# Kernel tuning notes

Hardware: AMD Instinct MI355X
Metric: run time of the kernel (lower is better)

Reference implementation:

```python
import jax, jax.numpy as jnp
import numpy as np

DN = ('NCHW', 'OIHW', 'NCHW')

def conv(x, w, b, stride=1, pad=0):
    y = jax.lax.conv_general_dilated(x, w, (stride, stride), ((pad, pad), (pad, pad)), dimension_numbers=DN)
    return y + b[None, :, None, None]

def maxpool(x, k, s):
    return jax.lax.reduce_window(x, -jnp.inf, jax.lax.max, (1, 1, k, k), (1, 1, s, s), 'VALID')

def bilinear_resize(x, oh, ow):
    # torch F.interpolate(mode='bilinear', align_corners=False)
    H, W = x.shape[2], x.shape[3]
    def grid(n_in, n_out):
        c = (jnp.arange(n_out, dtype=x.dtype) + 0.5) * (n_in / n_out) - 0.5
        c = jnp.clip(c, 0.0, n_in - 1)
        lo = jnp.floor(c).astype(jnp.int32)
        hi = jnp.minimum(lo + 1, n_in - 1)
        return lo, hi, c - lo
    r0, r1, wr = grid(H, oh)
    c0, c1, wc = grid(W, ow)
    top = x[:, :, r0, :] * (1 - wr)[None, None, :, None] + x[:, :, r1, :] * wr[None, None, :, None]
    return top[:, :, :, c0] * (1 - wc) + top[:, :, :, c1] * wc

def setup_inputs():
    key = jax.random.key(0)
    ks = jax.random.split(key, 18)
    s = 0.02
    d = {}
    d['x'] = jax.random.normal(ks[0], (16, 3, 448, 448), jnp.float32)
    d['w1'] = jax.random.normal(ks[1], (64, 3, 7, 7), jnp.float32) * s
    d['b1'] = jax.random.normal(ks[2], (64,), jnp.float32) * s
    d['w3'] = jax.random.normal(ks[3], (192, 64, 3, 3), jnp.float32) * s
    d['b3'] = jax.random.normal(ks[4], (192,), jnp.float32) * s
    d['w4'] = jax.random.normal(ks[5], (256, 192, 3, 3), jnp.float32) * s
    d['b4'] = jax.random.normal(ks[6], (256,), jnp.float32) * s
    d['w7'] = jax.random.normal(ks[7], (512, 256, 2, 2), jnp.float32) * s
    d['b7'] = jax.random.normal(ks[8], (512,), jnp.float32) * s
    d['w8'] = jax.random.normal(ks[9], (1024, 512, 2, 2), jnp.float32) * s
    d['b8'] = jax.random.normal(ks[10], (1024,), jnp.float32) * s
    d['wu'] = jax.random.normal(ks[11], (1024, 1024, 2, 2), jnp.float32) * s
    d['bu'] = jax.random.normal(ks[12], (1024,), jnp.float32) * s
    d['lc_w'] = jax.random.normal(ks[13], (1024, 256, 7, 7, 3, 3), jnp.float32) * s
    d['lc_b'] = jax.random.normal(ks[14], (256, 7, 7), jnp.float32) * s
    d['fc_w'] = jax.random.normal(ks[15], (4949, 12544), jnp.float32) * s  # S*S*(C+B*5)=7*7*101
    d['fc_b'] = jax.random.normal(ks[16], (4949,), jnp.float32) * s
    return d

def reference(x, w1, b1, w3, b3, w4, b4, w7, b7, w8, b8, wu, bu, lc_w, lc_b, fc_w, fc_b):
    x = conv(x, w1, b1, 2, 3)        # [B,64,224,224]
    x = maxpool(x, 2, 2)             # 112
    x = conv(x, w3, b3, 1, 1)        # [B,192,112,112]
    x = maxpool(x, 2, 2)             # 56
    x = conv(x, w4, b4)              # [B,256,54,54]
    x = maxpool(x, 2, 2)             # 27
    # CombinedNet backbone not defined in source listing: identity (256->256)
    x = conv(x, w7, b7)              # [B,512,26,26]
    x = maxpool(x, 2, 2)             # 13
    x = conv(x, w8, b8)              # [B,1024,12,12]
    x = conv(x, wu, bu)              # 11 (ultblock applied twice, shared weights)
    x = conv(x, wu, bu)              # 10
    x = maxpool(x, 5, 4)             # [B,1024,2,2]
    x = x[:, :, :14, :14]
    x = bilinear_resize(x, 7, 7)     # [B,1024,7,7]
    # LocallyConnected2d(1024,256,7,7,k=3,s=1,p=1) without materializing the unfold*weight product
    B = x.shape[0]
    xp = jnp.pad(x, ((0, 0), (0, 0), (1, 1), (1, 1)))
    patches = jnp.stack([xp[:, :, i:i + 7, j:j + 7] for i in range(3) for j in range(3)], axis=2)
    patches = patches.reshape(B, 1024, 3, 3, 7, 7)  # [B,C,kh,kw,H,W]
    y = jnp.einsum('bcijhw,cohwij->bohw', patches, lc_w) + lc_b[None]
    y = jnp.where(y > 0, y, 0.1 * y)  # LeakyReLU(0.1)
    # Dropout(p=0.5) is identity at inference; Linear
    y = y.reshape(B, -1) @ fc_w.T + fc_b  # [B,4949]
    return y.reshape(B, 7, 7, 101)
```

## Files before the change

kernel.cpp:

```cpp
#include <hip/hip_runtime.h>

#define UNR _Pragma("unroll")

typedef __attribute__((ext_vector_type(8))) short short8v;
typedef __attribute__((ext_vector_type(4))) float f32x4;

__device__ __forceinline__ ushort f2bf(float f) {
    union { float f; unsigned u; } x; x.f = f;
    unsigned r = (x.u + 0x7fffu + ((x.u >> 16) & 1u)) >> 16;
    return (ushort)r;
}
__device__ __forceinline__ float bf2f(ushort u) {
    union { unsigned u; float f; } x; x.u = ((unsigned)u) << 16;
    return x.f;
}

__device__ __forceinline__ void gll16(const ushort* gp, ushort* lp) {
    __builtin_amdgcn_global_load_lds(
        (const __attribute__((address_space(1))) unsigned int*)(const void*)gp,
        (__attribute__((address_space(3))) unsigned int*)(void*)lp, 16, 0, 0);
}

template<int Wp,int Hp,int OW,int OH,int WpN,int HpN,int PADN,int CN,int WAVES>
__global__ __launch_bounds__(WAVES*64)
void convc1(const ushort* __restrict__ Xp, const ushort* __restrict__ Wb,
            const float* __restrict__ bias, ushort* __restrict__ Yp)
{
    constexpr int CIN = 4, STRIDE = 2, NSTEP = 7;
    constexpr int POW = OW/2, POH = OH/2;
    constexpr int NTOT = 16*POW*POH*4;

    const int lane = (int)threadIdx.x & 63;
    const int wave = (int)threadIdx.x >> 6;
    const int n0   = (blockIdx.y*WAVES + wave) * 64;
    const int lm   = lane & 15;
    const int lk   = lane >> 4;

    int ns[4];
    unsigned boff[4];
    UNR for (int nf=0; nf<4; ++nf) {
        int n = n0 + nf*16 + lm;
        if (n > NTOT-1) n = NTOT-1;
        ns[nf] = n;
        int q = n & 3, pp = n >> 2;
        int px = pp % POW; int t = pp / POW;
        int py = t % POH;  int b = t / POH;
        int oy = 2*py + (q>>1), ox = 2*px + (q&1);
        boff[nf] = ((unsigned)(b*Hp + oy*STRIDE)*Wp + (unsigned)(ox*STRIDE))*CIN
                 + 8u*lk;
    }

    f32x4 acc[4][4];
    UNR for (int i=0;i<4;++i) UNR for (int j=0;j<4;++j) acc[i][j] = f32x4{0.f,0.f,0.f,0.f};

    auto ldfr = [&](int s, short8v (&a)[4], short8v (&bf)[4]) {
        const unsigned xoff = (unsigned)(s*Wp*CIN);
        UNR for (int mf=0; mf<4; ++mf)
            a[mf] = *(const short8v*)(Wb + (unsigned)((s*4 + mf)<<9) + (unsigned)lane*8);
        UNR for (int nf=0; nf<4; ++nf)
            bf[nf] = *(const short8v*)(Xp + boff[nf] + xoff);
    };
    auto dm = [&](short8v (&a)[4], short8v (&bf)[4]) {
        UNR for (int mf=0; mf<4; ++mf)
            UNR for (int nf=0; nf<4; ++nf)
                acc[mf][nf] = __builtin_amdgcn_mfma_f32_16x16x32_bf16(
                                  a[mf], bf[nf], acc[mf][nf], 0, 0, 0);
    };

    short8v aA[4], bA[4], aB[4], bB[4];
    ldfr(0, aA, bA);
    for (int sb = 0; sb < NSTEP; sb += 2) {
        if (sb+1 < NSTEP) ldfr(sb+1, aB, bB);
        dm(aA, bA);
        if (sb+2 < NSTEP) ldfr(sb+2, aA, bA);
        if (sb+1 < NSTEP) dm(aB, bB);
    }

    UNR for (int mf=0; mf<4; ++mf) {
        const int co = mf*16 + 4*lk;
        f32x4 bi = *(const f32x4*)(bias + co);
        UNR for (int nf=0; nf<4; ++nf) {
            f32x4 v = acc[mf][nf];
            UNR for (int r=0;r<4;++r) {
                float t2 = v[r] + bi[r];
                t2 = fmaxf(t2, __shfl_xor(t2, 1, 64));
                t2 = fmaxf(t2, __shfl_xor(t2, 2, 64));
                v[r] = t2;
            }
            if ((lane & 3) == 0 && (n0 + nf*16 + lm) < NTOT) {
                int pp = ns[nf] >> 2;
                int px = pp % POW; int t2 = pp / POW;
                int py = t2 % POH; int b = t2 / POH;
                unsigned off = ((unsigned)(b*HpN + py + PADN)*WpN
                                + (unsigned)(px + PADN))*CN + co;
                ushort4 s; s.x=f2bf(v[0]); s.y=f2bf(v[1]); s.z=f2bf(v[2]); s.w=f2bf(v[3]);
                *(ushort4*)(Yp + off) = s;
            }
        }
    }
}

template<int CIN,int K,int STRIDE,int Wp,int Hp,int OW,int OH,int COUT,
         bool POOL,int WpN,int HpN,int PADN,int CN,int MT,int NT,int SPLITS,
         int LINX=0,int LINY=0>
__global__ __launch_bounds__(256)
void convt(const ushort* __restrict__ Xp, const ushort* __restrict__ Wb,
           const float* __restrict__ bias, ushort* __restrict__ Yp,
           float* __restrict__ part)
{
    static_assert(MT*NT == 4, "4 waves");
    constexpr int POW = OW/2, POH = OH/2;
    constexpr int NTOT = POOL ? 16*POW*POH*4 : 16*OW*OH;
    constexpr int NCH = CIN/32, NSTEP = K*K*NCH;
    constexpr int SPS = NSTEP/SPLITS;
    constexpr int CA = MT*4, CB = NT*4, CPW = MT + NT;

    int bx, by;
    if constexpr (LINX > 0) {
        constexpr int CHUNK = LINX*LINY/8;
        int bid = (int)blockIdx.x;
        int p = (bid & 7)*CHUNK + (bid >> 3);
        bx = p % LINX; by = p / LINX;
    } else {
        bx = (int)blockIdx.x; by = (int)blockIdx.y;
    }

    const int t    = (int)threadIdx.x;
    const int lane = t & 63;
    const int w    = t >> 6;
    const int mr   = w / NT, nc = w % NT;
    const int cy0  = bx * MT;
    const int n0b  = by * (NT*64);
    const int nw0  = n0b + nc*64;
    const int lm   = lane & 15, lk = lane >> 4;
    const int s0   = blockIdx.z * SPS, sE = s0 + SPS;

    __shared__ __align__(1024) ushort Ab[2][CA*512];
    __shared__ __align__(1024) ushort Bb[2][CB*512];

    auto nmap = [&](int n, int& b, int& oy, int& ox) {
        if (n > NTOT-1) n = NTOT-1;
        if constexpr (POOL) {
            int q = n & 3, pp = n >> 2;
            int px = pp % POW; int tt = pp / POW;
            int py = tt % POH;  b = tt / POH;
            oy = 2*py + (q>>1); ox = 2*px + (q&1);
        } else {
            ox = n % OW; int tt = n / OW; oy = tt % OH; b = tt / OH;
        }
    };

    int ns[4];
    UNR for (int nf=0; nf<4; ++nf) {
        int n = nw0 + nf*16 + lm;
        if (n > NTOT-1) n = NTOT-1;
        ns[nf] = n;
    }

    unsigned bsrc[CPW];
    UNR for (int j=0; j<CPW; ++j) {
        int q = w*CPW + j;
        if (q >= CA) {
            int bq = q - CA;
            int n = n0b + bq*16 + (lane >> 2);
            int b, oy, ox; nmap(n, b, oy, ox);
            bsrc[j] = ((unsigned)(b*Hp + oy*STRIDE)*Wp + (unsigned)(ox*STRIDE))*CIN
                    + (unsigned)(lane & 3)*8u;
        } else bsrc[j] = 0;
    }

    auto xoffs = [&](int s) -> unsigned {
        int c0  = (s % NCH)*32;
        int kxy = s / NCH;
        int kx  = kxy % K, ky = kxy / K;
        return (unsigned)((ky*Wp + kx)*CIN + c0);
    };
    auto stage = [&](int s, int buf) {
        const unsigned xoff = xoffs(s);
        UNR for (int j=0; j<CPW; ++j) {
            int q = w*CPW + j;
            if (q < CA) {
                const ushort* src = Wb
                    + ((size_t)(((cy0 + (q>>2))*NSTEP + s)*4 + (q&3)) << 9)
                    + (unsigned)lane*8;
                gll16(src, &Ab[buf][(unsigned)q*512u + (unsigned)lane*8u]);
            } else {
                gll16(Xp + bsrc[j] + xoff,
                      &Bb[buf][(unsigned)(q-CA)*512u + (unsigned)lane*8u]);
            }
        }
    };

    f32x4 acc[4][4];
    UNR for (int i=0;i<4;++i) UNR for (int j=0;j<4;++j) acc[i][j] = f32x4{0.f,0.f,0.f,0.f};

    auto compute = [&](int buf) {
        short8v a[4], bf[4];
        UNR for (int mf=0; mf<4; ++mf)
            a[mf] = *(const short8v*)&Ab[buf][(unsigned)((mr*4+mf)*64 + lane)*8u];
        UNR for (int nf=0; nf<4; ++nf)
            bf[nf] = *(const short8v*)&Bb[buf][(unsigned)((nc*64 + nf*16 + lm)*4 + lk)*8u];
        __builtin_amdgcn_s_setprio(1);
        UNR for (int mf=0; mf<4; ++mf)
            UNR for (int nf=0; nf<4; ++nf)
                acc[mf][nf] = __builtin_amdgcn_mfma_f32_16x16x32_bf16(
                                  a[mf], bf[nf], acc[mf][nf], 0, 0, 0);
        __builtin_amdgcn_s_setprio(0);
    };

    stage(s0, 0);
    __syncthreads();
    int buf = 0;
    for (int s = s0; s < sE; ++s) {
        if (s+1 < sE) stage(s+1, buf^1);
        compute(buf);
        __syncthreads();
        buf ^= 1;
    }

    UNR for (int mf=0; mf<4; ++mf) {
        const int co = (cy0 + mr)*64 + mf*16 + 4*lk;
        if constexpr (SPLITS > 1) {
            UNR for (int nf=0; nf<4; ++nf) {
                if ((nw0 + nf*16 + lm) < NTOT)
                    *(f32x4*)(part + ((size_t)blockIdx.z*NTOT + ns[nf])*COUT + co)
                        = acc[mf][nf];
            }
        } else {
            f32x4 bi = *(const f32x4*)(bias + co);
            UNR for (int nf=0; nf<4; ++nf) {
                f32x4 v = acc[mf][nf];
                UNR for (int r=0;r<4;++r) v[r] += bi[r];
                if constexpr (POOL) {
                    UNR for (int r=0;r<4;++r) {
                        float tt = v[r];
                        tt = fmaxf(tt, __shfl_xor(tt, 1, 64));
                        tt = fmaxf(tt, __shfl_xor(tt, 2, 64));
                        v[r] = tt;
                    }
                    if ((lane & 3) == 0 && (nw0 + nf*16 + lm) < NTOT) {
                        int pp = ns[nf] >> 2;
                        int px = pp % POW; int t2 = pp / POW;
                        int py = t2 % POH; int b = t2 / POH;
                        unsigned off = ((unsigned)(b*HpN + py + PADN)*WpN
                                        + (unsigned)(px + PADN))*CN + co;
                        ushort4 s2; s2.x=f2bf(v[0]); s2.y=f2bf(v[1]); s2.z=f2bf(v[2]); s2.w=f2bf(v[3]);
                        *(ushort4*)(Yp + off) = s2;
                    }
                } else {
                    if ((nw0 + nf*16 + lm) < NTOT) {
                        int n = ns[nf];
                        int ox = n % OW; int t2 = n / OW; int oy = t2 % OH; int b = t2 / OH;
                        unsigned off = ((unsigned)(b*HpN + oy)*WpN + (unsigned)ox)*CN + co;
                        ushort4 s2; s2.x=f2bf(v[0]); s2.y=f2bf(v[1]); s2.z=f2bf(v[2]); s2.w=f2bf(v[3]);
                        *(ushort4*)(Yp + off) = s2;
                    }
                }
            }
        }
    }
}

template<int COUT,int OW,int OH,int WpN,int HpN,int CN,int SPLITS>
__global__ void kreduce(const float* __restrict__ part, const float* __restrict__ bias,
                        ushort* __restrict__ Yp) {
    constexpr int NTOT = 16*OW*OH;
    int idx = blockIdx.x*256 + (int)threadIdx.x;
    if (idx >= NTOT*COUT) return;
    int co = idx % COUT; int n = idx / COUT;
    float sum = 0.f;
    UNR for (int ks=0; ks<SPLITS; ++ks)
        sum += part[((size_t)ks*NTOT + n)*COUT + co];
    sum += bias[co];
    int ox = n % OW; int t = n / OW; int oy = t % OH; int b = t / OH;
    Yp[((unsigned)(b*HpN + oy)*WpN + (unsigned)ox)*CN + co] = f2bf(sum);
}

__global__ void x1build(const float* __restrict__ x, ushort* __restrict__ X1) {
    int idx = blockIdx.x*256 + (int)threadIdx.x;
    int xx = idx % 456; int t = idx/456; int y = t % 456; int b = t/456;
    ushort4 s; s.x = 0; s.y = 0; s.z = 0; s.w = 0;
    if (xx >= 3 && xx < 451 && y >= 3 && y < 451) {
        const float* px = x + ((size_t)b*3*448 + (y-3))*448 + (xx-3);
        s.x = f2bf(px[0]); s.y = f2bf(px[200704]); s.z = f2bf(px[401408]);
    }
    *(ushort4*)(X1 + ((unsigned)(b*456 + y)*456 + (unsigned)xx)*4) = s;
}

__global__ void x3ring(ushort* __restrict__ X3) {
    int idx = blockIdx.x*256 + (int)threadIdx.x;
    if (idx >= 462848) return;
    int b = idx / 28928; int j = idx % 28928;
    unsigned off;
    if (j < 14592) {
        int r = j / 7296; int rem = j % 7296;
        int y = r ? 113 : 0;
        off = ((unsigned)(b*114 + y)*114)*64u + (unsigned)rem;
    } else {
        int j2 = j - 14592;
        int y = 1 + j2/128;
        int rem = j2 % 128;
        int xx = (rem >> 6) ? 113 : 0;
        off = (((unsigned)(b*114 + y)*114) + (unsigned)xx)*64u + (unsigned)(rem & 63);
    }
    X3[off] = 0;
}

__global__ void wcvt1(const float* __restrict__ w, ushort* __restrict__ o) {
    int idx = blockIdx.x*256 + (int)threadIdx.x;
    if (idx >= 14336) return;
    int e = idx & 7; int t = idx >> 3;
    int lane = t & 63; t >>= 6;
    int mf = t & 3; int s = t >> 2;
    int co = mf*16 + (lane & 15);
    int cc = (lane >> 4)*8 + e;
    int kx = cc >> 2, ci = cc & 3;
    float v = 0.f;
    if (kx < 7 && ci < 3) v = w[(((size_t)co*3 + ci)*7 + s)*7 + kx];
    o[idx] = f2bf(v);
}

template<int CIN,int K,int COUT>
__global__ void wcvt(const float* __restrict__ w, ushort* __restrict__ o) {
    constexpr int NCH = CIN/32, NSTEP = K*K*NCH;
    int idx = blockIdx.x*256 + (int)threadIdx.x;
    if (idx >= COUT*K*K*CIN) return;
    int e = idx & 7; int t = idx >> 3;
    int lane = t & 63; t >>= 6;
    int mf = t & 3; t >>= 2;
    int s = t % NSTEP; int cy = t / NSTEP;
    int co = cy*64 + mf*16 + (lane & 15);
    int kxy = s / NCH, ch = s % NCH;
    int ci = ch*32 + (lane >> 4)*8 + e;
    int ky = kxy / K, kx = kxy % K;
    o[idx] = f2bf(w[(((size_t)co*CIN + ci)*K + ky)*K + kx]);
}

__global__ void pool54_k(const ushort* __restrict__ in, float* __restrict__ out) {
    int idx = blockIdx.x*256 + (int)threadIdx.x;
    int c = idx & 1023; int t = idx >> 10; int q = t & 3; int b = t >> 2;
    int i = q >> 1, j = q & 1;
    float m = -1e30f;
    UNR for (int r=0;r<5;++r)
        UNR for (int cc=0;cc<5;++cc)
            m = fmaxf(m, bf2f(in[(((unsigned)(b*10 + i*4+r))*10 + (unsigned)(j*4+cc))*1024 + c]));
    out[((size_t)(b*1024 + c))*4 + q] = m;
}

__device__ __forceinline__ void bigrid(int k, int& lo, float& f) {
    float c = ((float)k + 0.5f) * (2.0f/7.0f) - 0.5f;
    c = fminf(fmaxf(c, 0.f), 1.f);
    float fl = floorf(c);
    lo = (int)fl;
    f = c - fl;
}

__global__ void buildPb(const float* __restrict__ pp, ushort* __restrict__ Pb) {
    int idx = blockIdx.x*256 + (int)threadIdx.x;
    int k = idx & 15;
    int c = (idx >> 4) & 1023;
    int r = idx >> 14;
    int b = r & 15; int hw = r >> 4;
    float val = 0.f;
    if (k < 9) {
        int i = k/3, j = k%3;
        int h = hw/7, w2 = hw%7;
        int rr = h + i - 1, cc = w2 + j - 1;
        if (rr>=0 && rr<7 && cc>=0 && cc<7) {
            int rlo; float rf; bigrid(rr, rlo, rf);
            int clo; float cf; bigrid(cc, clo, cf);
            int rhi = min(rlo+1,1), chi = min(clo+1,1);
            const float* qq = pp + ((size_t)(b*1024 + c))*4;
            float v00=qq[rlo*2+clo], v01=qq[rlo*2+chi], v10=qq[rhi*2+clo], v11=qq[rhi*2+chi];
            float top = v00*(1.f-cf) + v01*cf;
            float bot = v10*(1.f-cf) + v11*cf;
            val = top*(1.f-rf) + bot*rf;
        }
    }
    Pb[idx] = f2bf(val);
}

__global__ __launch_bounds__(256)
void lconv_fused(const float* __restrict__ lcw, const ushort* __restrict__ Pb,
                 float* __restrict__ part) {
    const int bid = (int)blockIdx.x;
    const int xcd = bid & 7;
    const int i   = bid >> 3;
    const int hw  = i % 49;
    const int ks  = xcd + 8*(i/49);
    const int t   = (int)threadIdx.x;
    const int lane = t & 63, w = t >> 6;
    const int lm = lane & 15, lk = lane >> 4;
    const int c0 = ks*64;

    __shared__ ushort A[2][8192];

    auto ldreg = [&](int cc, float (&w9)[2][9]) {
        const int cb = c0 + cc*2;
        UNR for (int cl=0; cl<2; ++cl) {
            const float* src = lcw + ((size_t)(cb+cl)*256 + (unsigned)(w*64+lane))*441
                             + hw*9;
            __builtin_memcpy(w9[cl], src, 36);
        }
    };
    auto wrlds = [&](int buf, float (&w9)[2][9]) {
        UNR for (int cl=0; cl<2; ++cl) {
            int rem = cl*256 + w*64 + lane;
            ushort u[16];
            UNR for (int k=0;k<8;++k) u[k]=f2bf(w9[cl][k]);
            u[8]=f2bf(w9[cl][8]);
            UNR for (int k=9;k<16;++k) u[k]=0;
            *(short8v*)&A[buf][(unsigned)rem*8u] = *(short8v*)&u[0];
            *(short8v*)&A[buf][4096u + (unsigned)rem*8u] = *(short8v*)&u[8];
        }
    };

    f32x4 acc[4];
    UNR for (int q=0;q<4;++q) acc[q] = f32x4{0.f,0.f,0.f,0.f};

    const ushort* Bb = Pb + (size_t)(hw*16 + lm)*16384 + ks*1024 + lk*8;
    const int arow = (lk&1)*512 + (lk>>1)*256 + w*64 + lm;

    auto mmac = [&](int buf, int cc) {
        short8v bv = *(const short8v*)(Bb + cc*32);
        UNR for (int mf = 0; mf < 4; ++mf) {
            short8v av = *(const short8v*)&A[buf][(unsigned)(arow + mf*16)*8u];
            acc[mf] = __builtin_amdgcn_mfma_f32_16x16x32_bf16(av, bv, acc[mf], 0,0,0);
        }
    };

    float wA[2][9], wB[2][9];
    ldreg(0, wA);
    wrlds(0, wA);
    ldreg(1, wB);
    for (int cc = 0; cc < 32; cc += 2) {
        mmac(0, cc);
        wrlds(1, wB);
        if (cc+2 < 32) ldreg(cc+2, wA);
        mmac(1, cc+1);
        if (cc+2 < 32) {
            wrlds(0, wA);
            if (cc+3 < 32) ldreg(cc+3, wB);
        }
    }

    UNR for (int mf=0; mf<4; ++mf)
        UNR for (int r=0;r<4;++r) {
            int o = w*64 + mf*16 + 4*lk + r;
            part[(((size_t)ks*49 + hw)*256 + o)*16 + lm] = acc[mf][r];
        }
}

__global__ void lreduce2(const float* __restrict__ part, const float* __restrict__ lcb,
                         float* __restrict__ yact) {
    int idx = blockIdx.x*256 + (int)threadIdx.x;
    int b = idx & 15; int o = (idx >> 4) & 255; int hw = idx >> 12;
    float sum = 0.f;
    UNR for (int ks=0; ks<16; ++ks)
        sum += part[(((size_t)ks*49 + hw)*256 + o)*16 + b];
    sum += lcb[o*49 + hw];
    float v = (sum > 0.f) ? sum : 0.1f*sum;
    yact[b*12544 + o*49 + hw] = v;
}

__global__ __launch_bounds__(256)
void fc_k(const float* __restrict__ act, const float* __restrict__ fw,
          const float* __restrict__ fb, float* __restrict__ out) {
    __shared__ float alds[16][256];
    __shared__ float red[4][4][16];
    const int t = (int)threadIdx.x;
    const int o0 = blockIdx.x*4;
    float acc[4][16];
    UNR for (int oo=0;oo<4;++oo) UNR for (int b=0;b<16;++b) acc[oo][b]=0.f;

    for (int k0=0; k0<12544; k0+=256) {
        __syncthreads();
        UNR for (int b=0;b<16;++b) alds[b][t] = act[b*12544 + k0 + t];
        __syncthreads();
        float wv[4];
        UNR for (int oo=0;oo<4;++oo) {
            int o = o0+oo;
            wv[oo] = (o < 4949) ? fw[(size_t)o*12544 + k0 + t] : 0.f;
        }
        UNR for (int b=0;b<16;++b) {
            float av = alds[b][t];
            UNR for (int oo=0;oo<4;++oo) acc[oo][b] = fmaf(wv[oo], av, acc[oo][b]);
        }
    }
    UNR for (int oo=0;oo<4;++oo)
        UNR for (int b=0;b<16;++b) {
            float v = acc[oo][b];
            UNR for (int off=32; off; off>>=1) v += __shfl_xor(v, off, 64);
            acc[oo][b] = v;
        }
    const int wave = t>>6, lane = t&63;
    if (lane == 0)
        UNR for (int oo=0;oo<4;++oo)
            UNR for (int b=0;b<16;++b) red[wave][oo][b] = acc[oo][b];
    __syncthreads();
    if (t < 64) {
        int oo = t>>4, b = t&15;
        float v = red[0][oo][b]+red[1][oo][b]+red[2][oo][b]+red[3][oo][b];
        int o = o0+oo;
        if (o < 4949) out[b*4949 + o] = v + fb[o];
    }
}

extern "C" void kernel_launch(void* const* d_in, const int* in_sizes, int n_in,
                              void* d_out, int out_size, void* d_ws, size_t ws_size,
                              hipStream_t stream) {
    const float* x   = (const float*)d_in[0];
    const float* w1  = (const float*)d_in[1];
    const float* b1  = (const float*)d_in[2];
    const float* w3  = (const float*)d_in[3];
    const float* b3  = (const float*)d_in[4];
    const float* w4  = (const float*)d_in[5];
    const float* b4  = (const float*)d_in[6];
    const float* w7  = (const float*)d_in[7];
    const float* b7  = (const float*)d_in[8];
    const float* w8  = (const float*)d_in[9];
    const float* b8  = (const float*)d_in[10];
    const float* wu  = (const float*)d_in[11];
    const float* bu  = (const float*)d_in[12];
    const float* lcw = (const float*)d_in[13];
    const float* lcb = (const float*)d_in[14];
    const float* fw  = (const float*)d_in[15];
    const float* fb  = (const float*)d_in[16];
    float* out = (float*)d_out;

    char* base = (char*)d_ws;
    auto alloc = [&](size_t bytes) { char* p = base; base += (bytes + 255) & ~(size_t)255; return p; };
    ushort* X1  = (ushort*)alloc(16u*456*456*4*2);
    ushort* X3  = (ushort*)alloc(16u*114*114*64*2);
    ushort* X4  = (ushort*)alloc(16u*56*56*192*2);
    ushort* X7  = (ushort*)alloc(16u*27*27*256*2);
    ushort* X8  = (ushort*)alloc(16u*13*13*512*2);
    ushort* XU1 = (ushort*)alloc(16u*12*12*1024*2);
    ushort* XU2 = (ushort*)alloc(16u*11*11*1024*2);
    ushort* XU3 = (ushort*)alloc(16u*10*10*1024*2);
    ushort* W1b = (ushort*)alloc(64u*224*2);
    ushort* W3b = (ushort*)alloc(192u*576*2);
    ushort* W4b = (ushort*)alloc(256u*1728*2);
    ushort* W7b = (ushort*)alloc(512u*1024*2);
    ushort* W8b = (ushort*)alloc(1024u*2048*2);
    ushort* WUb = (ushort*)alloc(1024u*4096*2);
    float*  pp  = (float*)alloc(16u*1024*4*4);
    ushort* Pb  = (ushort*)alloc((size_t)49*16*16384*2);
    float*  part = (float*)alloc((size_t)16*49*256*16*4);
    float*  partK = (float*)alloc((size_t)4*2304*1024*4);
    float*  yact = (float*)X7;

    x1build<<<12996, 256, 0, stream>>>(x, X1);
    x3ring<<<1808, 256, 0, stream>>>(X3);
    wcvt1<<<56, 256, 0, stream>>>(w1, W1b);
    wcvt<64,3,192><<<432, 256, 0, stream>>>(w3, W3b);
    wcvt<192,3,256><<<1728, 256, 0, stream>>>(w4, W4b);
    wcvt<256,2,512><<<2048, 256, 0, stream>>>(w7, W7b);
    wcvt<512,2,1024><<<8192, 256, 0, stream>>>(w8, W8b);
    wcvt<1024,2,1024><<<16384, 256, 0, stream>>>(wu, WUb);

    convc1<456,456,224,224,114,114,1,64, 4>
        <<<dim3(1,3136), 256, 0, stream>>>(X1, W1b, b1, X3);
    convt<64,3,1,114,114,112,112,192, true,56,56,0,192, 1,4,1, 3,784>
        <<<2352, 256, 0, stream>>>(X3, W3b, b3, X4, nullptr);
    convt<192,3,1,56,56,54,54,256, true,27,27,0,256, 2,2,1>
        <<<dim3(2,365,1), 256, 0, stream>>>(X4, W4b, b4, X7, nullptr);
    convt<256,2,1,27,27,26,26,512, true,13,13,0,512, 2,2,1>
        <<<dim3(4,85,1), 256, 0, stream>>>(X7, W7b, b7, X8, nullptr);
    convt<512,2,1,13,13,12,12,1024, false,12,12,0,1024, 2,2,4>
        <<<dim3(8,18,4), 256, 0, stream>>>(X8, W8b, nullptr, nullptr, partK);
    kreduce<1024,12,12,12,12,1024,4><<<9216, 256, 0, stream>>>(partK, b8, XU1);
    convt<1024,2,1,12,12,11,11,1024, false,11,11,0,1024, 2,2,4>
        <<<dim3(8,16,4), 256, 0, stream>>>(XU1, WUb, nullptr, nullptr, partK);
    kreduce<1024,11,11,11,11,1024,4><<<7744, 256, 0, stream>>>(partK, bu, XU2);
    convt<1024,2,1,11,11,10,10,1024, false,10,10,0,1024, 2,2,4>
        <<<dim3(8,13,4), 256, 0, stream>>>(XU2, WUb, nullptr, nullptr, partK);
    kreduce<1024,10,10,10,10,1024,4><<<6400, 256, 0, stream>>>(partK, bu, XU3);

    pool54_k<<<256, 256, 0, stream>>>(XU3, pp);
    buildPb<<<50176, 256, 0, stream>>>(pp, Pb);
    lconv_fused<<<784, 256, 0, stream>>>(lcw, Pb, part);
    lreduce2<<<784, 256, 0, stream>>>(part, lcb, yact);
    fc_k<<<1238, 256, 0, stream>>>(yact, fw, fb, out);
}
```

Measured before the change: 784.9 us.

## Vectorize split-K reductions, XCD-aware block remap, and re-layout conv B staging

The split-K reduction kernels (kreduce, lreduce2) now have each thread handle four outputs using 16-byte vector loads, with launch sizes cut to match, which lowers load instruction count and thread overhead. A general XCD-balanced block-id remap replaces the fixed chunking and is now also applied to the conv4 and conv7 launches, which switch to 1D grids, to improve L2 locality per XCD. The B-tile staging in convt changes its lane-to-pixel/channel mapping so LDS fragment reads become contiguous per lane. This alters the LDS layout for B, which must stay consistent with the MFMA operand format, and it may change bank-conflict and global-coalescing behaviour.

Result: slower. 818.0 us (+4.2%).

```diff
diff --git a/kernel.cpp b/kernel.cpp
--- a/kernel.cpp
+++ b/kernel.cpp
@@ -19,6 +19,12 @@
     __builtin_amdgcn_global_load_lds(
         (const __attribute__((address_space(1))) unsigned int*)(const void*)gp,
         (__attribute__((address_space(3))) unsigned int*)(void*)lp, 16, 0, 0);
+}
+
+__device__ __forceinline__ int xcdmap(int bid, int nwg) {
+    int q = nwg >> 3, r = nwg & 7;
+    int xcd = bid & 7, i = bid >> 3;
+    return (xcd < r) ? (xcd*(q+1) + i) : (r*(q+1) + (xcd-r)*q + i);
 }
 
 template<int Wp,int Hp,int OW,int OH,int WpN,int HpN,int PADN,int CN,int WAVES>
@@ -117,9 +123,7 @@
 
     int bx, by;
     if constexpr (LINX > 0) {
-        constexpr int CHUNK = LINX*LINY/8;
-        int bid = (int)blockIdx.x;
-        int p = (bid & 7)*CHUNK + (bid >> 3);
+        int p = xcdmap((int)blockIdx.x, LINX*LINY);
         bx = p % LINX; by = p / LINX;
     } else {
         bx = (int)blockIdx.x; by = (int)blockIdx.y;
@@ -162,10 +166,10 @@
         int q = w*CPW + j;
         if (q >= CA) {
             int bq = q - CA;
-            int n = n0b + bq*16 + (lane >> 2);
+            int n = n0b + bq*16 + (lane & 15);
             int b, oy, ox; nmap(n, b, oy, ox);
             bsrc[j] = ((unsigned)(b*Hp + oy*STRIDE)*Wp + (unsigned)(ox*STRIDE))*CIN
-                    + (unsigned)(lane & 3)*8u;
+                    + (unsigned)(lane >> 4)*8u;
         } else bsrc[j] = 0;
     }
 
@@ -199,7 +203,7 @@
         UNR for (int mf=0; mf<4; ++mf)
             a[mf] = *(const short8v*)&Ab[buf][(unsigned)((mr*4+mf)*64 + lane)*8u];
         UNR for (int nf=0; nf<4; ++nf)
-            bf[nf] = *(const short8v*)&Bb[buf][(unsigned)((nc*64 + nf*16 + lm)*4 + lk)*8u];
+            bf[nf] = *(const short8v*)&Bb[buf][(unsigned)(((nc*4+nf)*64) + lane)*8u];
         __builtin_amdgcn_s_setprio(1);
         UNR for (int mf=0; mf<4; ++mf)
             UNR for (int nf=0; nf<4; ++nf)
@@ -265,15 +269,21 @@
 __global__ void kreduce(const float* __restrict__ part, const float* __restrict__ bias,
                         ushort* __restrict__ Yp) {
     constexpr int NTOT = 16*OW*OH;
-    int idx = blockIdx.x*256 + (int)threadIdx.x;
-    if (idx >= NTOT*COUT) return;
-    int co = idx % COUT; int n = idx / COUT;
-    float sum = 0.f;
-    UNR for (int ks=0; ks<SPLITS; ++ks)
-        sum += part[((size_t)ks*NTOT + n)*COUT + co];
-    sum += bias[co];
+    constexpr int C4 = COUT/4;
+    int idx = blockIdx.x*256 + (int)threadIdx.x;
+    if (idx >= NTOT*C4) return;
+    int c4 = (idx % C4)*4; int n = idx / C4;
+    f32x4 sum = *(const f32x4*)(part + ((size_t)n)*COUT + c4);
+    UNR for (int ks=1; ks<SPLITS; ++ks) {
+        f32x4 p = *(const f32x4*)(part + ((size_t)ks*NTOT + n)*COUT + c4);
+        UNR for (int r=0;r<4;++r) sum[r] += p[r];
+    }
+    f32x4 bi = *(const f32x4*)(bias + c4);
     int ox = n % OW; int t = n / OW; int oy = t % OH; int b = t / OH;
-    Yp[((unsigned)(b*HpN + oy)*WpN + (unsigned)ox)*CN + co] = f2bf(sum);
+    ushort4 s;
+    s.x = f2bf(sum[0]+bi[0]); s.y = f2bf(sum[1]+bi[1]);
+    s.z = f2bf(sum[2]+bi[2]); s.w = f2bf(sum[3]+bi[3]);
+    *(ushort4*)(Yp + ((unsigned)(b*HpN + oy)*WpN + (unsigned)ox)*CN + c4) = s;
 }
 
 __global__ void x1build(const float* __restrict__ x, ushort* __restrict__ X1) {
@@ -454,13 +464,17 @@
 __global__ void lreduce2(const float* __restrict__ part, const float* __restrict__ lcb,
                          float* __restrict__ yact) {
     int idx = blockIdx.x*256 + (int)threadIdx.x;
-    int b = idx & 15; int o = (idx >> 4) & 255; int hw = idx >> 12;
-    float sum = 0.f;
-    UNR for (int ks=0; ks<16; ++ks)
-        sum += part[(((size_t)ks*49 + hw)*256 + o)*16 + b];
-    sum += lcb[o*49 + hw];
-    float v = (sum > 0.f) ? sum : 0.1f*sum;
-    yact[b*12544 + o*49 + hw] = v;
+    int b4 = (idx & 3)*4; int o = (idx >> 2) & 255; int hw = idx >> 10;
+    f32x4 sum = *(const f32x4*)(part + (((size_t)hw)*256 + o)*16 + b4);
+    UNR for (int ks=1; ks<16; ++ks) {
+        f32x4 p = *(const f32x4*)(part + (((size_t)ks*49 + hw)*256 + o)*16 + b4);
+        UNR for (int r=0;r<4;++r) sum[r] += p[r];
+    }
+    float bias = lcb[o*49 + hw];
+    UNR for (int r=0;r<4;++r) {
+        float s = sum[r] + bias;
+        yact[(b4+r)*12544 + o*49 + hw] = (s > 0.f) ? s : 0.1f*s;
+    }
 }
 
 __global__ __launch_bounds__(256)
@@ -563,23 +577,23 @@
         <<<dim3(1,3136), 256, 0, stream>>>(X1, W1b, b1, X3);
     convt<64,3,1,114,114,112,112,192, true,56,56,0,192, 1,4,1, 3,784>
         <<<2352, 256, 0, stream>>>(X3, W3b, b3, X4, nullptr);
-    convt<192,3,1,56,56,54,54,256, true,27,27,0,256, 2,2,1>
-        <<<dim3(2,365,1), 256, 0, stream>>>(X4, W4b, b4, X7, nullptr);
-    convt<256,2,1,27,27,26,26,512, true,13,13,0,512, 2,2,1>
-        <<<dim3(4,85,1), 256, 0, stream>>>(X7, W7b, b7, X8, nullptr);
+    convt<192,3,1,56,56,54,54,256, true,27,27,0,256, 2,2,1, 2,365>
+        <<<730, 256, 0, stream>>>(X4, W4b, b4, X7, nullptr);
+    convt<256,2,1,27,27,26,26,512, true,13,13,0,512, 2,2,1, 4,85>
+        <<<340, 256, 0, stream>>>(X7, W7b, b7, X8, nullptr);
     convt<512,2,1,13,13,12,12,1024, false,12,12,0,1024, 2,2,4>
         <<<dim3(8,18,4), 256, 0, stream>>>(X8, W8b, nullptr, nullptr, partK);
-    kreduce<1024,12,12,12,12,1024,4><<<9216, 256, 0, stream>>>(partK, b8, XU1);
+    kreduce<1024,12,12,12,12,1024,4><<<2304, 256, 0, stream>>>(partK, b8, XU1);
     convt<1024,2,1,12,12,11,11,1024, false,11,11,0,1024, 2,2,4>
         <<<dim3(8,16,4), 256, 0, stream>>>(XU1, WUb, nullptr, nullptr, partK);
-    kreduce<1024,11,11,11,11,1024,4><<<7744, 256, 0, stream>>>(partK, bu, XU2);
+    kreduce<1024,11,11,11,11,1024,4><<<1936, 256, 0, stream>>>(partK, bu, XU2);
     convt<1024,2,1,11,11,10,10,1024, false,10,10,0,1024, 2,2,4>
         <<<dim3(8,13,4), 256, 0, stream>>>(XU2, WUb, nullptr, nullptr, partK);
-    kreduce<1024,10,10,10,10,1024,4><<<6400, 256, 0, stream>>>(partK, bu, XU3);
+    kreduce<1024,10,10,10,10,1024,4><<<1600, 256, 0, stream>>>(partK, bu, XU3);
 
     pool54_k<<<256, 256, 0, stream>>>(XU3, pp);
     buildPb<<<50176, 256, 0, stream>>>(pp, Pb);
     lconv_fused<<<784, 256, 0, stream>>>(lcw, Pb, part);
-    lreduce2<<<784, 256, 0, stream>>>(part, lcb, yact);
+    lreduce2<<<196, 256, 0, stream>>>(part, lcb, yact);
     fc_k<<<1238, 256, 0, stream>>>(yact, fw, fb, out);
 }
```
